# Performance work log

Measured on AMD Instinct MI355X. Metric: run time of the kernel, lower is better.

The kernel has to match this reference:

```python
import jax, jax.numpy as jnp
import numpy as np

IN = 4096   # input_size * 2 (is_bichar)
H = 2048    # hidden_size
C = 4096    # number of lexicon inputs


def setup_inputs() -> dict:
    key = jax.random.key(0)
    ks = jax.random.split(key, 12)
    s = 0.02
    return {
        "x": jax.random.normal(ks[0], (1, IN), jnp.float32),
        "c_input": jax.random.normal(ks[1], (C, H), jnp.float32),
        "h0": jax.random.normal(ks[2], (1, H), jnp.float32),
        "c0": jax.random.normal(ks[3], (1, H), jnp.float32),
        "W_ih": jax.random.normal(ks[4], (4 * H, IN), jnp.float32) * s,
        "b_ih": jnp.zeros((4 * H,), jnp.float32),
        "W_hh": jax.random.normal(ks[5], (4 * H, H), jnp.float32) * s,
        "b_hh": jnp.zeros((4 * H,), jnp.float32),
        "aW_ih": jax.random.normal(ks[6], (H, IN), jnp.float32) * s,
        "ab_ih": jnp.zeros((H,), jnp.float32),
        "aW_hh": jax.random.normal(ks[7], (H, H), jnp.float32) * s,
        "ab_hh": jnp.zeros((H,), jnp.float32),
    }


def reference(x, c_input, h0, c0, W_ih, b_ih, W_hh, b_hh, aW_ih, ab_ih, aW_hh, ab_hh):
    # gate pre-activations: [1, 4H]
    lstm_vec = x @ W_ih.T + b_ih + h0 @ W_hh.T + b_hh
    i, f, o, g = jnp.split(lstm_vec, 4, axis=1)
    i = jax.nn.sigmoid(i)
    f = jax.nn.sigmoid(f + 1.0)  # computed but unused when lexicon is non-empty (faithful)
    g = jnp.tanh(g)
    o = jax.nn.sigmoid(o)
    # alpha over lexicon entries: [C, H] (x-projection broadcasts over C)
    alpha = jax.nn.sigmoid(x @ aW_ih.T + ab_ih + c_input @ aW_hh.T + ab_hh)
    # exp-normalize over the (C+1) candidates per hidden unit
    w = jnp.exp(jnp.concatenate([i, alpha], axis=0))  # [C+1, H]
    w = w / w.sum(axis=0)
    merge = jnp.concatenate([g, c_input], axis=0)  # [C+1, H]
    c1 = (merge * w).sum(axis=0, keepdims=True)  # [1, H]
    h1 = o * jnp.tanh(c1)
    return h1, c1
```

## Files before the change

kernel.cpp:

```cpp
#include <hip/hip_runtime.h>
#include <hip/hip_bf16.h>
#include <cstdint>

#define HDIM 2048
#define INDIM 4096
#define CDIM 4096
#define KDIM 2048

typedef __attribute__((ext_vector_type(4))) int int4v;

__device__ __forceinline__ void gload16(const void* g, void* l) {
  __builtin_amdgcn_global_load_lds(
      (const __attribute__((address_space(1))) void*)g,
      (__attribute__((address_space(3))) void*)l, 16, 0, 0);
}

__global__ __launch_bounds__(256) void k_prep(
    const float* __restrict__ c_input, const float* __restrict__ aW_hh,
    int8_t* __restrict__ a8, int8_t* __restrict__ b8,
    float* __restrict__ dAs, float* __restrict__ dBs,
    const float* __restrict__ x, const float* __restrict__ h0,
    const float* __restrict__ W_ih, const float* __restrict__ b_ih,
    const float* __restrict__ W_hh, const float* __restrict__ b_hh,
    const float* __restrict__ aW_ih, const float* __restrict__ ab_ih,
    const float* __restrict__ ab_hh,
    float* __restrict__ i_sig, float* __restrict__ o_sig,
    float* __restrict__ g_tanh, float* __restrict__ xa2,
    float* __restrict__ accz) {
  const int t = threadIdx.x;
  const int wid = t >> 6, lane = t & 63;

  if (blockIdx.x < CDIM + HDIM) {
    if (blockIdx.x == 0) {
#pragma unroll
      for (int i = 0; i < 16; ++i) accz[i * 256 + t] = 0.f;
    }
    const int row = blockIdx.x;
    const float* src; int8_t* dst; float* dsc; int r;
    if (row < CDIM) { src = c_input; dst = a8; dsc = dAs; r = row; }
    else            { src = aW_hh;  dst = b8; dsc = dBs; r = row - CDIM; }
    const float4* s4 = (const float4*)(src + (size_t)r * KDIM);
    const float4 v0 = s4[t * 2], v1 = s4[t * 2 + 1];
    float am = fmaxf(fmaxf(fmaxf(fabsf(v0.x), fabsf(v0.y)),
                           fmaxf(fabsf(v0.z), fabsf(v0.w))),
                     fmaxf(fmaxf(fabsf(v1.x), fabsf(v1.y)),
                           fmaxf(fabsf(v1.z), fabsf(v1.w))));
#pragma unroll
    for (int off = 32; off > 0; off >>= 1) am = fmaxf(am, __shfl_xor(am, off));
    __shared__ float wmax[4];
    if (lane == 0) wmax[wid] = am;
    __syncthreads();
    am = fmaxf(fmaxf(wmax[0], wmax[1]), fmaxf(wmax[2], wmax[3]));
    am = fmaxf(am, 1e-20f);
    const float inv = 127.0f / am;
    const float vv[8] = {v0.x, v0.y, v0.z, v0.w, v1.x, v1.y, v1.z, v1.w};
    uint32_t p0 = 0, p1 = 0;
#pragma unroll
    for (int i = 0; i < 4; ++i)
      p0 |= (uint32_t)(__float2int_rn(vv[i] * inv) & 0xFF) << (i * 8);
#pragma unroll
    for (int i = 0; i < 4; ++i)
      p1 |= (uint32_t)(__float2int_rn(vv[4 + i] * inv) & 0xFF) << (i * 8);
    *(uint2*)(dst + (size_t)r * KDIM + t * 8) = make_uint2(p0, p1);
    if (t == 0) dsc[r] = am * (1.0f / 127.0f);
    return;
  }

  const int vr = (blockIdx.x - (CDIM + HDIM)) * 4 + wid;
  const int typ = vr >> 11;
  const int h = vr & (HDIM - 1);
  float sum = 0.f;
  if (typ < 3) {
    const int grow = (typ == 0) ? h : (typ == 1) ? (2 * HDIM + h) : (3 * HDIM + h);
    const float4* wr4 = (const float4*)(W_ih + (size_t)grow * INDIM);
    const float4* x4 = (const float4*)x;
#pragma unroll
    for (int it = 0; it < INDIM / 256; ++it) {
      float4 w = wr4[it * 64 + lane], xv = x4[it * 64 + lane];
      sum += w.x * xv.x + w.y * xv.y + w.z * xv.z + w.w * xv.w;
    }
    const float4* wh4 = (const float4*)(W_hh + (size_t)grow * HDIM);
    const float4* h4 = (const float4*)h0;
#pragma unroll
    for (int it = 0; it < HDIM / 256; ++it) {
      float4 w = wh4[it * 64 + lane], hv = h4[it * 64 + lane];
      sum += w.x * hv.x + w.y * hv.y + w.z * hv.z + w.w * hv.w;
    }
#pragma unroll
    for (int off = 32; off > 0; off >>= 1) sum += __shfl_down(sum, off);
    if (lane == 0) {
      float z = sum + b_ih[grow] + b_hh[grow];
      if (typ == 0)      i_sig[h] = 1.f / (1.f + expf(-z));
      else if (typ == 1) o_sig[h] = 1.f / (1.f + expf(-z));
      else               g_tanh[h] = tanhf(z);
    }
  } else {
    const float4* wr4 = (const float4*)(aW_ih + (size_t)h * INDIM);
    const float4* x4 = (const float4*)x;
#pragma unroll
    for (int it = 0; it < INDIM / 256; ++it) {
      float4 w = wr4[it * 64 + lane], xv = x4[it * 64 + lane];
      sum += w.x * xv.x + w.y * xv.y + w.z * xv.z + w.w * xv.w;
    }
#pragma unroll
    for (int off = 32; off > 0; off >>= 1) sum += __shfl_down(sum, off);
    if (lane == 0) xa2[h] = sum + ab_ih[h] + ab_hh[h];
  }
}

__global__ __launch_bounds__(256) void k_gemm_i8(
    const int8_t* __restrict__ A, const int8_t* __restrict__ B,
    const float* __restrict__ dAs, const float* __restrict__ dBs,
    const float* __restrict__ c_in, const float* __restrict__ xa2,
    float* __restrict__ acc_se, float* __restrict__ acc_sce) {
  __shared__ uint8_t As[16384];
  __shared__ uint8_t Bs[16384];
  const int t = threadIdx.x;
  const int lane = t & 63, wid = t >> 6;
  const int wr = wid >> 1, wc = wid & 1;
  const int l15 = lane & 15, l4 = lane >> 4;
  const int bm = blockIdx.x & 31, bn = blockIdx.x >> 5;
  const int m0 = bm * 128, n0 = bn * 128;

  int4v acc[4][4] = {};

  const int trow = t >> 3;
  const int tcol = ((t & 7) * 16) ^ ((trow & 7) << 4);
  const int8_t* Arow = A + (size_t)(m0 + trow) * KDIM + tcol;
  const int8_t* Brow = B + (size_t)(n0 + trow) * KDIM + tcol;

  for (int k0 = 0; k0 < KDIM; k0 += 128) {
#pragma unroll
    for (int qq = 0; qq < 4; ++qq) {
      gload16(Arow + (size_t)qq * 32 * KDIM + k0, As + qq * 4096 + t * 16);
      gload16(Brow + (size_t)qq * 32 * KDIM + k0, Bs + qq * 4096 + t * 16);
    }
    __syncthreads();
    int4v alo[4], ahi[4], blo[4], bhi[4];
#pragma unroll
    for (int m = 0; m < 4; ++m) {
      const int r = wr * 64 + m * 16 + l15;
      const int swz = (r & 7) << 4;
      alo[m] = *(const int4v*)(As + r * 128 + ((l4 * 16) ^ swz));
      ahi[m] = *(const int4v*)(As + r * 128 + ((64 + l4 * 16) ^ swz));
    }
#pragma unroll
    for (int n = 0; n < 4; ++n) {
      const int r = wc * 64 + n * 16 + l15;
      const int swz = (r & 7) << 4;
      blo[n] = *(const int4v*)(Bs + r * 128 + ((l4 * 16) ^ swz));
      bhi[n] = *(const int4v*)(Bs + r * 128 + ((64 + l4 * 16) ^ swz));
    }
#pragma unroll
    for (int m = 0; m < 4; ++m)
#pragma unroll
      for (int n = 0; n < 4; ++n) {
        acc[m][n] = __builtin_amdgcn_mfma_i32_16x16x64_i8(alo[m], blo[n], acc[m][n], 0, 0, 0);
        acc[m][n] = __builtin_amdgcn_mfma_i32_16x16x64_i8(ahi[m], bhi[n], acc[m][n], 0, 0, 0);
      }
    __syncthreads();
  }

#pragma unroll
  for (int n = 0; n < 4; ++n) {
    const int hcol = n0 + wc * 64 + n * 16 + l15;
    const float xa = xa2[hcol];
    const float db = dBs[hcol];
    float se = 0.f, sce = 0.f;
#pragma unroll
    for (int m = 0; m < 4; ++m) {
      const int jbase = m0 + wr * 64 + m * 16 + l4 * 4;
#pragma unroll
      for (int rr = 0; rr < 4; ++rr) {
        const float sc = dAs[jbase + rr] * db;
        float z = (float)acc[m][n][rr] * sc + xa;
        float s = 1.f / (1.f + __expf(-z));
        float e = __expf(s);
        se += e;
        sce += c_in[(size_t)(jbase + rr) * HDIM + hcol] * e;
      }
    }
    se += __shfl_xor(se, 16); se += __shfl_xor(se, 32);
    sce += __shfl_xor(sce, 16); sce += __shfl_xor(sce, 32);
    if (l4 == 0) {
      atomicAdd(&acc_se[hcol], se);
      atomicAdd(&acc_sce[hcol], sce);
    }
  }
}

__global__ __launch_bounds__(256) void k_final(
    const float* __restrict__ i_sig, const float* __restrict__ o_sig,
    const float* __restrict__ g_tanh, const float* __restrict__ acc_se,
    const float* __restrict__ acc_sce, float* __restrict__ out) {
  int h = blockIdx.x * 256 + threadIdx.x;
  if (h >= HDIM) return;
  float wi = expf(i_sig[h]);
  float tot = acc_se[h] + wi;
  float c1 = (acc_sce[h] + g_tanh[h] * wi) / tot;
  float h1 = o_sig[h] * tanhf(c1);
  out[h] = h1;
  out[HDIM + h] = c1;
}

extern "C" void kernel_launch(void* const* d_in, const int* in_sizes, int n_in,
                              void* d_out, int out_size, void* d_ws, size_t ws_size,
                              hipStream_t stream) {
  const float* x     = (const float*)d_in[0];
  const float* c_inp = (const float*)d_in[1];
  const float* h0    = (const float*)d_in[2];
  const float* W_ih  = (const float*)d_in[4];
  const float* b_ih  = (const float*)d_in[5];
  const float* W_hh  = (const float*)d_in[6];
  const float* b_hh  = (const float*)d_in[7];
  const float* aW_ih = (const float*)d_in[8];
  const float* ab_ih = (const float*)d_in[9];
  const float* aW_hh = (const float*)d_in[10];
  const float* ab_hh = (const float*)d_in[11];
  float* out = (float*)d_out;

  char* ws = (char*)d_ws;
  int8_t* a8 = (int8_t*)ws;
  int8_t* b8 = a8 + (size_t)CDIM * KDIM;
  float* dAs = (float*)(b8 + (size_t)HDIM * KDIM);
  float* dBs = dAs + CDIM;
  float* fb  = dBs + HDIM;
  float* i_sig   = fb;
  float* o_sig   = fb + HDIM;
  float* g_tanh  = fb + 2 * HDIM;
  float* xa2     = fb + 3 * HDIM;
  float* acc_se  = fb + 4 * HDIM;
  float* acc_sce = fb + 5 * HDIM;

  k_prep<<<CDIM + HDIM + 4 * HDIM / 4, 256, 0, stream>>>(
      c_inp, aW_hh, a8, b8, dAs, dBs,
      x, h0, W_ih, b_ih, W_hh, b_hh, aW_ih, ab_ih, ab_hh,
      i_sig, o_sig, g_tanh, xa2, acc_se);
  k_gemm_i8<<<(CDIM / 128) * (HDIM / 128), 256, 0, stream>>>(
      a8, b8, dAs, dBs, c_inp, xa2, acc_se, acc_sce);
  k_final<<<(HDIM + 255) / 256, 256, 0, stream>>>(i_sig, o_sig, g_tanh,
                                                  acc_se, acc_sce, out);
}
```

Baseline: 72.40 us.

## Double-buffer int8 GEMM LDS tiles and restructure prep kernel to warp-per-row

The int8 MFMA GEMM now uses two LDS buffers per operand, so the next K tile's global-to-LDS loads are issued before computing on the current one, overlapping memory latency with MFMA work. Launch bounds request two blocks per CU. The quantization prep now assigns one row per wavefront instead of one per block, which removes the shared-memory reduction and barrier and cuts the prep grid. The GEMV paths batch eight float4 loads before their FMAs to raise memory-level parallelism. Doubling LDS to 64KB per block may limit occupancy.

```diff
diff --git a/kernel.cpp b/kernel.cpp
--- a/kernel.cpp
+++ b/kernel.cpp
@@ -30,61 +30,71 @@
   const int t = threadIdx.x;
   const int wid = t >> 6, lane = t & 63;
 
-  if (blockIdx.x < CDIM + HDIM) {
+  if (blockIdx.x < 1536) {
     if (blockIdx.x == 0) {
 #pragma unroll
       for (int i = 0; i < 16; ++i) accz[i * 256 + t] = 0.f;
     }
-    const int row = blockIdx.x;
+    const int row = blockIdx.x * 4 + wid;
     const float* src; int8_t* dst; float* dsc; int r;
     if (row < CDIM) { src = c_input; dst = a8; dsc = dAs; r = row; }
     else            { src = aW_hh;  dst = b8; dsc = dBs; r = row - CDIM; }
     const float4* s4 = (const float4*)(src + (size_t)r * KDIM);
-    const float4 v0 = s4[t * 2], v1 = s4[t * 2 + 1];
-    float am = fmaxf(fmaxf(fmaxf(fabsf(v0.x), fabsf(v0.y)),
-                           fmaxf(fabsf(v0.z), fabsf(v0.w))),
-                     fmaxf(fmaxf(fabsf(v1.x), fabsf(v1.y)),
-                           fmaxf(fabsf(v1.z), fabsf(v1.w))));
+    float4 v[8];
+#pragma unroll
+    for (int it = 0; it < 8; ++it) v[it] = s4[it * 64 + lane];
+    float am = 0.f;
+#pragma unroll
+    for (int it = 0; it < 8; ++it)
+      am = fmaxf(am, fmaxf(fmaxf(fabsf(v[it].x), fabsf(v[it].y)),
+                           fmaxf(fabsf(v[it].z), fabsf(v[it].w))));
 #pragma unroll
     for (int off = 32; off > 0; off >>= 1) am = fmaxf(am, __shfl_xor(am, off));
-    __shared__ float wmax[4];
-    if (lane == 0) wmax[wid] = am;
-    __syncthreads();
-    am = fmaxf(fmaxf(wmax[0], wmax[1]), fmaxf(wmax[2], wmax[3]));
     am = fmaxf(am, 1e-20f);
     const float inv = 127.0f / am;
-    const float vv[8] = {v0.x, v0.y, v0.z, v0.w, v1.x, v1.y, v1.z, v1.w};
-    uint32_t p0 = 0, p1 = 0;
-#pragma unroll
-    for (int i = 0; i < 4; ++i)
-      p0 |= (uint32_t)(__float2int_rn(vv[i] * inv) & 0xFF) << (i * 8);
-#pragma unroll
-    for (int i = 0; i < 4; ++i)
-      p1 |= (uint32_t)(__float2int_rn(vv[4 + i] * inv) & 0xFF) << (i * 8);
-    *(uint2*)(dst + (size_t)r * KDIM + t * 8) = make_uint2(p0, p1);
-    if (t == 0) dsc[r] = am * (1.0f / 127.0f);
+    uint32_t* qd = (uint32_t*)(dst + (size_t)r * KDIM);
+#pragma unroll
+    for (int it = 0; it < 8; ++it) {
+      uint32_t p = (uint32_t)(__float2int_rn(v[it].x * inv) & 0xFF)
+                 | ((uint32_t)(__float2int_rn(v[it].y * inv) & 0xFF) << 8)
+                 | ((uint32_t)(__float2int_rn(v[it].z * inv) & 0xFF) << 16)
+                 | ((uint32_t)(__float2int_rn(v[it].w * inv) & 0xFF) << 24);
+      qd[it * 64 + lane] = p;
+    }
+    if (lane == 0) dsc[r] = am * (1.0f / 127.0f);
     return;
   }
 
-  const int vr = (blockIdx.x - (CDIM + HDIM)) * 4 + wid;
+  const int vr = (blockIdx.x - 1536) * 4 + wid;
   const int typ = vr >> 11;
   const int h = vr & (HDIM - 1);
   float sum = 0.f;
+  const float4* x4 = (const float4*)x;
   if (typ < 3) {
     const int grow = (typ == 0) ? h : (typ == 1) ? (2 * HDIM + h) : (3 * HDIM + h);
     const float4* wr4 = (const float4*)(W_ih + (size_t)grow * INDIM);
-    const float4* x4 = (const float4*)x;
-#pragma unroll
-    for (int it = 0; it < INDIM / 256; ++it) {
-      float4 w = wr4[it * 64 + lane], xv = x4[it * 64 + lane];
-      sum += w.x * xv.x + w.y * xv.y + w.z * xv.z + w.w * xv.w;
+#pragma unroll
+    for (int g = 0; g < 2; ++g) {
+      float4 w[8];
+#pragma unroll
+      for (int it = 0; it < 8; ++it) w[it] = wr4[(g * 8 + it) * 64 + lane];
+#pragma unroll
+      for (int it = 0; it < 8; ++it) {
+        float4 xv = x4[(g * 8 + it) * 64 + lane];
+        sum += w[it].x * xv.x + w[it].y * xv.y + w[it].z * xv.z + w[it].w * xv.w;
+      }
     }
     const float4* wh4 = (const float4*)(W_hh + (size_t)grow * HDIM);
     const float4* h4 = (const float4*)h0;
-#pragma unroll
-    for (int it = 0; it < HDIM / 256; ++it) {
-      float4 w = wh4[it * 64 + lane], hv = h4[it * 64 + lane];
-      sum += w.x * hv.x + w.y * hv.y + w.z * hv.z + w.w * hv.w;
+    {
+      float4 w[8];
+#pragma unroll
+      for (int it = 0; it < 8; ++it) w[it] = wh4[it * 64 + lane];
+#pragma unroll
+      for (int it = 0; it < 8; ++it) {
+        float4 hv = h4[it * 64 + lane];
+        sum += w[it].x * hv.x + w[it].y * hv.y + w[it].z * hv.z + w[it].w * hv.w;
+      }
     }
 #pragma unroll
     for (int off = 32; off > 0; off >>= 1) sum += __shfl_down(sum, off);
@@ -96,11 +106,16 @@
     }
   } else {
     const float4* wr4 = (const float4*)(aW_ih + (size_t)h * INDIM);
-    const float4* x4 = (const float4*)x;
-#pragma unroll
-    for (int it = 0; it < INDIM / 256; ++it) {
-      float4 w = wr4[it * 64 + lane], xv = x4[it * 64 + lane];
-      sum += w.x * xv.x + w.y * xv.y + w.z * xv.z + w.w * xv.w;
+#pragma unroll
+    for (int g = 0; g < 2; ++g) {
+      float4 w[8];
+#pragma unroll
+      for (int it = 0; it < 8; ++it) w[it] = wr4[(g * 8 + it) * 64 + lane];
+#pragma unroll
+      for (int it = 0; it < 8; ++it) {
+        float4 xv = x4[(g * 8 + it) * 64 + lane];
+        sum += w[it].x * xv.x + w[it].y * xv.y + w[it].z * xv.z + w[it].w * xv.w;
+      }
     }
 #pragma unroll
     for (int off = 32; off > 0; off >>= 1) sum += __shfl_down(sum, off);
@@ -108,13 +123,13 @@
   }
 }
 
-__global__ __launch_bounds__(256) void k_gemm_i8(
+__global__ __launch_bounds__(256, 2) void k_gemm_i8(
     const int8_t* __restrict__ A, const int8_t* __restrict__ B,
     const float* __restrict__ dAs, const float* __restrict__ dBs,
     const float* __restrict__ c_in, const float* __restrict__ xa2,
     float* __restrict__ acc_se, float* __restrict__ acc_sce) {
-  __shared__ uint8_t As[16384];
-  __shared__ uint8_t Bs[16384];
+  __shared__ uint8_t As[2][16384];
+  __shared__ uint8_t Bs[2][16384];
   const int t = threadIdx.x;
   const int lane = t & 63, wid = t >> 6;
   const int wr = wid >> 1, wc = wid & 1;
@@ -129,27 +144,35 @@
   const int8_t* Arow = A + (size_t)(m0 + trow) * KDIM + tcol;
   const int8_t* Brow = B + (size_t)(n0 + trow) * KDIM + tcol;
 
-  for (int k0 = 0; k0 < KDIM; k0 += 128) {
-#pragma unroll
-    for (int qq = 0; qq < 4; ++qq) {
-      gload16(Arow + (size_t)qq * 32 * KDIM + k0, As + qq * 4096 + t * 16);
-      gload16(Brow + (size_t)qq * 32 * KDIM + k0, Bs + qq * 4096 + t * 16);
-    }
-    __syncthreads();
+#define STAGE(buf, k0)                                                      \
+  do {                                                                      \
+    _Pragma("unroll")                                                       \
+    for (int qq = 0; qq < 4; ++qq) {                                        \
+      gload16(Arow + (size_t)qq * 32 * KDIM + (k0), As[buf] + qq * 4096 + t * 16); \
+      gload16(Brow + (size_t)qq * 32 * KDIM + (k0), Bs[buf] + qq * 4096 + t * 16); \
+    }                                                                       \
+  } while (0)
+
+  STAGE(0, 0);
+  __syncthreads();
+
+  int cur = 0;
+  for (int ti = 0; ti < KDIM / 128; ++ti) {
+    if (ti < KDIM / 128 - 1) STAGE(cur ^ 1, (ti + 1) * 128);
     int4v alo[4], ahi[4], blo[4], bhi[4];
 #pragma unroll
     for (int m = 0; m < 4; ++m) {
       const int r = wr * 64 + m * 16 + l15;
       const int swz = (r & 7) << 4;
-      alo[m] = *(const int4v*)(As + r * 128 + ((l4 * 16) ^ swz));
-      ahi[m] = *(const int4v*)(As + r * 128 + ((64 + l4 * 16) ^ swz));
+      alo[m] = *(const int4v*)(As[cur] + r * 128 + ((l4 * 16) ^ swz));
+      ahi[m] = *(const int4v*)(As[cur] + r * 128 + ((64 + l4 * 16) ^ swz));
     }
 #pragma unroll
     for (int n = 0; n < 4; ++n) {
       const int r = wc * 64 + n * 16 + l15;
       const int swz = (r & 7) << 4;
-      blo[n] = *(const int4v*)(Bs + r * 128 + ((l4 * 16) ^ swz));
-      bhi[n] = *(const int4v*)(Bs + r * 128 + ((64 + l4 * 16) ^ swz));
+      blo[n] = *(const int4v*)(Bs[cur] + r * 128 + ((l4 * 16) ^ swz));
+      bhi[n] = *(const int4v*)(Bs[cur] + r * 128 + ((64 + l4 * 16) ^ swz));
     }
 #pragma unroll
     for (int m = 0; m < 4; ++m)
@@ -159,7 +182,9 @@
         acc[m][n] = __builtin_amdgcn_mfma_i32_16x16x64_i8(ahi[m], bhi[n], acc[m][n], 0, 0, 0);
       }
     __syncthreads();
-  }
+    cur ^= 1;
+  }
+#undef STAGE
 
 #pragma unroll
   for (int n = 0; n < 4; ++n) {
@@ -232,7 +257,7 @@
   float* acc_se  = fb + 4 * HDIM;
   float* acc_sce = fb + 5 * HDIM;
 
-  k_prep<<<CDIM + HDIM + 4 * HDIM / 4, 256, 0, stream>>>(
+  k_prep<<<1536 + 2048, 256, 0, stream>>>(
       c_inp, aW_hh, a8, b8, dAs, dBs,
       x, h0, W_ih, b_ih, W_hh, b_hh, aW_ih, ab_ih, ab_hh,
       i_sig, o_sig, g_tanh, xa2, acc_se);
```

New measurement: 69.98 us. 1.03x faster.
